# Kernel tuning notes

Hardware: AMD Instinct MI355X
Metric: run time of the kernel (lower is better)

## Reference

```python
import jax, jax.numpy as jnp
import numpy as np

N = 7          # N_AGENTS (hardcoded in source)
H = 4          # n_heads
TOP_K = 3
EPS = 1e-5
NEG = -1.0e9


def _gat(x, W, a_src, a_dst, edge_mask):
    # x: (B,N,F), W: (F,H*Hd), a_src/a_dst: (H,Hd), edge_mask: (N,N)
    B = x.shape[0]
    Hd = a_src.shape[1]
    h = (x @ W).reshape(B, N, H, Hd)
    s_src = jnp.einsum('bnhd,hd->bnh', h, a_src)
    s_dst = jnp.einsum('bnhd,hd->bnh', h, a_dst)
    e = s_src[:, :, None, :] + s_dst[:, None, :, :]          # (B,N,N,H)
    e = jnp.where(e > 0, e, 0.2 * e)                          # LeakyReLU(0.2)
    m = edge_mask[None, :, :, None]
    e = e * m + (1.0 - m) * NEG
    if TOP_K < N:
        # k-th largest along axis=2 (ascending sort -> index N-TOP_K)
        thr = jnp.sort(e, axis=2)[:, :, N - TOP_K:N - TOP_K + 1, :]
        sm = (e >= thr).astype(e.dtype)
        e = e * sm + (1.0 - sm) * NEG
    alpha = jax.nn.softmax(e, axis=2)
    alpha = jnp.nan_to_num(alpha)
    out = jnp.einsum('bijh,bjhd->bihd', alpha, h).reshape(B, N, H * Hd)
    return out, alpha.mean(-1)


def _ln(x, w, b):
    mu = x.mean(-1, keepdims=True)
    var = ((x - mu) ** 2).mean(-1, keepdims=True)
    return (x - mu) / jnp.sqrt(var + EPS) * w + b


def _forward(node_feats, context, base_preds, regime_feats, edge_logits,
             W1, a_src1, a_dst1, W2, a_src2, a_dst2,
             ln1_w, ln1_b, ln2_w, ln2_b, skip_w, skip_b,
             base_w1, base_b1, base_w2, base_b2,
             reg_w1, reg_b1, reg_w2, reg_b2,
             gate_w1, gate_b1, gate_w2, gate_b2,
             res_w1, res_b1, res_w2, res_b2):
    B = node_feats.shape[0]
    eye = jnp.eye(N, dtype=edge_logits.dtype)
    edge_mask = jax.nn.sigmoid(edge_logits) * (1.0 - eye) + eye

    skip = node_feats @ skip_w + skip_b
    h1, _ = _gat(node_feats, W1, a_src1, a_dst1, edge_mask)
    h = jax.nn.relu(_ln(h1 + skip, ln1_w, ln1_b))
    h2, attn = _gat(h, W2, a_src2, a_dst2, edge_mask)
    h = jax.nn.relu(_ln(h2 + h, ln2_w, ln2_b))

    combined = jnp.concatenate([h.reshape(B, -1), context], axis=-1)
    w_base = jax.nn.softmax(jax.nn.relu(combined @ base_w1 + base_b1) @ base_w2 + base_b2, axis=-1)
    w_regime = jax.nn.softmax(jax.nn.relu(combined @ reg_w1 + reg_b1) @ reg_w2 + reg_b2, axis=-1)
    gate = jax.nn.sigmoid(jnp.tanh(regime_feats @ gate_w1 + gate_b1) @ gate_w2 + gate_b2)  # (B,1)
    weights = (1.0 - gate) * w_base + gate * w_regime
    pred = (weights * base_preds).sum(-1)
    residual = (jnp.tanh(combined @ res_w1 + res_b1) @ res_w2 + res_b2)[:, 0] * 0.05
    pred = jnp.maximum(pred + residual, 0.05)
    return pred, weights, gate, edge_mask, attn


def setup_inputs() -> dict:
    key = jax.random.key(0)
    B, F, C, HID, NB = 16384, 256, 128, 256, 2
    Hd = HID // H
    G = N * HID + C
    ks = iter(jax.random.split(key, 40))
    nrm = lambda shp, s: jax.random.normal(next(ks), shp, jnp.float32) * s
    d = {
        'node_feats': nrm((B, N, F), 1.0),
        'context': nrm((B, C), 1.0),
        'base_preds': jax.random.uniform(next(ks), (B, NB), jnp.float32),
        'regime_feats': nrm((B, 3), 1.0),
        'edge_logits': nrm((N, N), 0.1),
        'W1': nrm((F, HID), (2.0 / (F + HID)) ** 0.5),
        'a_src1': nrm((H, Hd), 0.1), 'a_dst1': nrm((H, Hd), 0.1),
        'W2': nrm((HID, HID), (1.0 / HID) ** 0.5),
        'a_src2': nrm((H, Hd), 0.1), 'a_dst2': nrm((H, Hd), 0.1),
        'ln1_w': jnp.ones((HID,), jnp.float32), 'ln1_b': jnp.zeros((HID,), jnp.float32),
        'ln2_w': jnp.ones((HID,), jnp.float32), 'ln2_b': jnp.zeros((HID,), jnp.float32),
        'skip_w': nrm((F, HID), (1.0 / F) ** 0.5), 'skip_b': jnp.zeros((HID,), jnp.float32),
        'base_w1': nrm((G, 32), (1.0 / G) ** 0.5), 'base_b1': jnp.zeros((32,), jnp.float32),
        'base_w2': nrm((32, NB), 0.1), 'base_b2': jnp.zeros((NB,), jnp.float32),
        'reg_w1': nrm((G, 32), (1.0 / G) ** 0.5), 'reg_b1': jnp.zeros((32,), jnp.float32),
        'reg_w2': nrm((32, NB), 0.1), 'reg_b2': jnp.zeros((NB,), jnp.float32),
        'gate_w1': nrm((3, 8), 0.5), 'gate_b1': jnp.zeros((8,), jnp.float32),
        'gate_w2': nrm((8, 1), 0.3), 'gate_b2': jnp.zeros((1,), jnp.float32),
        'res_w1': nrm((G, 16), (1.0 / G) ** 0.5), 'res_b1': jnp.zeros((16,), jnp.float32),
        'res_w2': nrm((16, 1), 0.2), 'res_b2': jnp.zeros((1,), jnp.float32),
    }
    return d


def reference(node_feats, context, base_preds, regime_feats, edge_logits,
              W1, a_src1, a_dst1, W2, a_src2, a_dst2,
              ln1_w, ln1_b, ln2_w, ln2_b, skip_w, skip_b,
              base_w1, base_b1, base_w2, base_b2,
              reg_w1, reg_b1, reg_w2, reg_b2,
              gate_w1, gate_b1, gate_w2, gate_b2,
              res_w1, res_b1, res_w2, res_b2):
    return _forward(node_feats, context, base_preds, regime_feats, edge_logits,
                    W1, a_src1, a_dst1, W2, a_src2, a_dst2,
                    ln1_w, ln1_b, ln2_w, ln2_b, skip_w, skip_b,
                    base_w1, base_b1, base_w2, base_b2,
                    reg_w1, reg_b1, reg_w2, reg_b2,
                    gate_w1, gate_b1, gate_w2, gate_b2,
                    res_w1, res_b1, res_w2, res_b2)
```

## Files before the change

### kernel.cpp

```cpp
#include <hip/hip_runtime.h>
#include <hip/hip_bf16.h>

typedef unsigned short u16;
typedef __attribute__((ext_vector_type(8))) short bfrag8;
typedef __attribute__((ext_vector_type(8))) unsigned short u16x8;
typedef __attribute__((ext_vector_type(4))) unsigned short u16x4;
typedef __attribute__((ext_vector_type(4))) float f32x4;

__device__ __forceinline__ float bf2f(u16 u) {
    union { unsigned int i; float f; } v; v.i = ((unsigned int)u) << 16; return v.f;
}
__device__ __forceinline__ u16 f2bf(float f) {
    union { __hip_bfloat16 h; u16 u; } cv;
    cv.h = __float2bfloat16(f);
    return cv.u;
}
__device__ __forceinline__ float fast_tanh(float x) {
    float e = __expf(2.f * x);
    return (e - 1.f) / (e + 1.f);
}

#define TILE_M 128
#define TILE_N 128
#define TILE_K 32

#define GLOAD_LDS16(g, l) \
    __builtin_amdgcn_global_load_lds( \
        (const __attribute__((address_space(1))) void*)(g), \
        (__attribute__((address_space(3))) void*)(l), 16, 0, 0)

template<int HAS_BIAS, int C_MODE, int NGUARD>
__global__ __launch_bounds__(256)
void gemm_k(const u16* __restrict__ A, const u16* __restrict__ Bt,
            const float* __restrict__ bias, void* __restrict__ Cp,
            int M, int N, int K, int lda, int ldc, int nt, int kchunk)
{
    __shared__ u16 As[2][TILE_M][TILE_K];
    __shared__ u16 Bs[2][TILE_N][TILE_K];

    const int nwg = gridDim.x;
    const int q = nwg >> 3, r = nwg & 7;
    const int xcd = blockIdx.x & 7, pos = blockIdx.x >> 3;
    const int wg = (xcd < r ? xcd * (q + 1) : r * (q + 1) + (xcd - r) * q) + pos;
    const int m0 = (wg / nt) * TILE_M;
    const int n0 = (wg % nt) * TILE_N;

    const int kc   = blockIdx.y;
    const int kbeg = kc * kchunk;
    const int kend = (kbeg + kchunk < K) ? kbeg + kchunk : K;

    const int t    = threadIdx.x;
    const int lane = t & 63;
    const int w    = t >> 6;
    const int wm   = (w >> 1) * 64;
    const int wn   = (w & 1) * 64;
    const int lr   = lane & 15;
    const int kg   = (lane >> 4) * 8;

    const int lrow = lane >> 2;
    const int lcol = (lane & 3) * 8;
    const u16* gA0 = A  + (size_t)(m0 + 32 * w + lrow) * lda + lcol;
    const u16* gA1 = gA0 + (size_t)16 * lda;
    const u16* gB0 = Bt + (size_t)(n0 + 32 * w + lrow) * K + lcol;
    const u16* gB1 = gB0 + (size_t)16 * K;
    char* lA = (char*)&As[0][0][0] + w * 2048;
    char* lB = (char*)&Bs[0][0][0] + w * 2048;

    f32x4 acc[4][4];
#pragma unroll
    for (int i = 0; i < 4; ++i)
#pragma unroll
        for (int j = 0; j < 4; ++j) acc[i][j] = (f32x4){0.f, 0.f, 0.f, 0.f};

#define ISSUE(bufo, k0v) { \
        GLOAD_LDS16(gA0 + (k0v), lA + (bufo)); \
        GLOAD_LDS16(gA1 + (k0v), lA + 1024 + (bufo)); \
        GLOAD_LDS16(gB0 + (k0v), lB + (bufo)); \
        GLOAD_LDS16(gB1 + (k0v), lB + 1024 + (bufo)); \
    }

    ISSUE(0, kbeg)
    int buf = 0;
    for (int k0 = kbeg; k0 < kend; k0 += TILE_K) {
        const bool more = (k0 + TILE_K) < kend;
        if (more) {
            ISSUE((buf ^ 1) * 8192, k0 + TILE_K);
            asm volatile("s_waitcnt vmcnt(4)" ::: "memory");
        } else {
            asm volatile("s_waitcnt vmcnt(0)" ::: "memory");
        }
        __syncthreads();

        bfrag8 af[4], bfr[4];
#pragma unroll
        for (int mi = 0; mi < 4; ++mi) af[mi]  = *(const bfrag8*)&As[buf][wm + mi * 16 + lr][kg];
#pragma unroll
        for (int ni = 0; ni < 4; ++ni) bfr[ni] = *(const bfrag8*)&Bs[buf][wn + ni * 16 + lr][kg];
#pragma unroll
        for (int mi = 0; mi < 4; ++mi)
#pragma unroll
            for (int ni = 0; ni < 4; ++ni)
                acc[mi][ni] = __builtin_amdgcn_mfma_f32_16x16x32_bf16(af[mi], bfr[ni], acc[mi][ni], 0, 0, 0);

        __syncthreads();
        buf ^= 1;
    }
#undef ISSUE

    float* Cf = (float*)Cp + (size_t)kc * M * ldc;
#pragma unroll
    for (int mi = 0; mi < 4; ++mi) {
#pragma unroll
        for (int ni = 0; ni < 4; ++ni) {
            int col = n0 + wn + ni * 16 + lr;
            if (!NGUARD || col < N) {
                int row = m0 + wm + mi * 16 + (lane >> 4) * 4;
                float bv = 0.f;
                if (HAS_BIAS && kc == 0) bv = bias[col];
#pragma unroll
                for (int rr = 0; rr < 4; ++rr) {
                    float v = acc[mi][ni][rr] + bv;
                    if (C_MODE == 0) ((u16*)Cp)[(size_t)(row + rr) * ldc + col] = f2bf(v);
                    else             Cf[(size_t)(row + rr) * ldc + col] = v;
                }
            }
        }
    }
}

__global__ __launch_bounds__(256)
void precast_k(const float* __restrict__ in, u16* __restrict__ out, int n8)
{
    int i = blockIdx.x * 256 + threadIdx.x;
    if (i >= n8) return;
    const float4* p = (const float4*)(in + (size_t)i * 8);
    float4 a = p[0], b = p[1];
    u16x8 v;
    v[0] = f2bf(a.x); v[1] = f2bf(a.y); v[2] = f2bf(a.z); v[3] = f2bf(a.w);
    v[4] = f2bf(b.x); v[5] = f2bf(b.y); v[6] = f2bf(b.z); v[7] = f2bf(b.w);
    *(u16x8*)(out + (size_t)i * 8) = v;
}

__global__ __launch_bounds__(256)
void score_k(const u16* __restrict__ hs, int ld,
             const float* __restrict__ a_src, const float* __restrict__ a_dst,
             float* __restrict__ scores, int Mrows)
{
    const int wid  = blockIdx.x * 4 + (threadIdx.x >> 6);
    const int lane = threadIdx.x & 63;
    if (wid >= Mrows) return;
    const u16* hp = hs + (size_t)wid * ld + lane * 4;
    u16x4 xv = *(const u16x4*)hp;
    float s1 = 0.f, s2 = 0.f;
#pragma unroll
    for (int k = 0; k < 4; ++k) {
        float x = bf2f(xv[k]);
        s1 = fmaf(x, a_src[lane * 4 + k], s1);
        s2 = fmaf(x, a_dst[lane * 4 + k], s2);
    }
#pragma unroll
    for (int off = 1; off < 16; off <<= 1) {
        s1 += __shfl_xor(s1, off);
        s2 += __shfl_xor(s2, off);
    }
    if ((lane & 15) == 0) {
        scores[(size_t)wid * 8 + (lane >> 4)] = s1;
        scores[(size_t)wid * 8 + 4 + (lane >> 4)] = s2;
    }
}

template<int WRITE_ATTN>
__global__ __launch_bounds__(256)
void alpha_k(const float* __restrict__ scores, const float* __restrict__ em2,
             float* __restrict__ alpha, float* __restrict__ attn_out)
{
    const int t = blockIdx.x * 256 + threadIdx.x;
    const int b = t >> 2;
    const int h = t & 3;

    float ssrc[7], sdst[7];
#pragma unroll
    for (int n = 0; n < 7; ++n) {
        ssrc[n] = scores[(size_t)(b * 7 + n) * 8 + h];
        sdst[n] = scores[(size_t)(b * 7 + n) * 8 + 4 + h];
    }

    float al[49];
#pragma unroll
    for (int i = 0; i < 7; ++i) {
        float e[7];
#pragma unroll
        for (int j = 0; j < 7; ++j) {
            float v = ssrc[i] + sdst[j];
            v = fmaxf(v, 0.2f * v);
            e[j] = fmaf(v, em2[(i * 7 + j) * 2], em2[(i * 7 + j) * 2 + 1]);
        }
        float a1 = -3e38f, b1 = -3e38f, c1 = -3e38f;
#pragma unroll
        for (int j = 0; j < 7; ++j) {
            float v = e[j];
            float t2 = fminf(a1, v); a1 = fmaxf(a1, v);
            float t3 = fminf(b1, t2); b1 = fmaxf(b1, t2);
            c1 = fmaxf(c1, t3);
        }
        float psum = 0.f;
        float p[7];
#pragma unroll
        for (int j = 0; j < 7; ++j) {
            float qv = (e[j] >= c1) ? __expf(e[j] - a1) : 0.f;
            p[j] = qv; psum += qv;
        }
        float inv = 1.f / psum;
#pragma unroll
        for (int j = 0; j < 7; ++j) al[i * 7 + j] = p[j] * inv;
    }

    float* ap = alpha + (size_t)t * 49;
#pragma unroll
    for (int j = 0; j < 49; ++j) ap[j] = al[j];

    if (WRITE_ATTN) {
#pragma unroll
        for (int j = 0; j < 49; ++j) {
            float m = al[j];
            m += __shfl_xor(m, 1);
            m += __shfl_xor(m, 2);
            if (h == 0) attn_out[(size_t)b * 49 + j] = 0.25f * m;
        }
    }
}

__global__ __launch_bounds__(256)
void gat_apply_k(const u16* __restrict__ hh, int ld_hh,
                 const u16* __restrict__ resid, int ld_res, int res_off,
                 const float* __restrict__ alpha,
                 const float* __restrict__ ln_w, const float* __restrict__ ln_b,
                 u16* __restrict__ outp, int out_bs)
{
    const int t = threadIdx.x;
    const int b = blockIdx.x * 4 + (t >> 6);
    const int l = t & 63;
    const int c = l * 4;
    const int h = l >> 4;
    const size_t rowbase = (size_t)b * 7;

    float hv[7][4];
#pragma unroll
    for (int n = 0; n < 7; ++n) {
        u16x4 qv = *(const u16x4*)&hh[(rowbase + n) * ld_hh + c];
#pragma unroll
        for (int k = 0; k < 4; ++k) hv[n][k] = bf2f(qv[k]);
    }

    const float* ap = alpha + ((size_t)b * 4 + h) * 49;
    float4 lw = *(const float4*)&ln_w[c];
    float4 lb = *(const float4*)&ln_b[c];

#pragma unroll
    for (int i = 0; i < 7; ++i) {
        float a0 = ap[i * 7 + 0], a1 = ap[i * 7 + 1], a2 = ap[i * 7 + 2],
              a3 = ap[i * 7 + 3], a4 = ap[i * 7 + 4], a5 = ap[i * 7 + 5],
              a6 = ap[i * 7 + 6];
        u16x4 rr = *(const u16x4*)&resid[(rowbase + i) * ld_res + res_off + c];
        float x[4];
#pragma unroll
        for (int k = 0; k < 4; ++k) {
            float pv = a0 * hv[0][k];
            pv = fmaf(a1, hv[1][k], pv);
            pv = fmaf(a2, hv[2][k], pv);
            pv = fmaf(a3, hv[3][k], pv);
            pv = fmaf(a4, hv[4][k], pv);
            pv = fmaf(a5, hv[5][k], pv);
            pv = fmaf(a6, hv[6][k], pv);
            x[k] = pv + bf2f(rr[k]);
        }
        float s1 = (x[0] + x[1]) + (x[2] + x[3]);
        float s2 = fmaf(x[0], x[0], x[1] * x[1]) + fmaf(x[2], x[2], x[3] * x[3]);
#pragma unroll
        for (int off = 32; off > 0; off >>= 1) {
            s1 += __shfl_xor(s1, off);
            s2 += __shfl_xor(s2, off);
        }
        float mu  = s1 * (1.f / 256.f);
        float var = fmaxf(s2 * (1.f / 256.f) - mu * mu, 0.f);
        float inv = rsqrtf(var + 1e-5f);
        u16x4 o;
        o[0] = f2bf(fmaxf((x[0] - mu) * inv * lw.x + lb.x, 0.f));
        o[1] = f2bf(fmaxf((x[1] - mu) * inv * lw.y + lb.y, 0.f));
        o[2] = f2bf(fmaxf((x[2] - mu) * inv * lw.z + lb.z, 0.f));
        o[3] = f2bf(fmaxf((x[3] - mu) * inv * lw.w + lb.w, 0.f));
        *(u16x4*)&outp[(size_t)b * out_bs + i * 256 + c] = o;
    }
}

__global__ __launch_bounds__(256)
void prep_k(const float* __restrict__ W1, const float* __restrict__ skip_w, const float* __restrict__ W2,
            const float* __restrict__ base_w1, const float* __restrict__ reg_w1, const float* __restrict__ res_w1,
            const float* __restrict__ skip_b, const float* __restrict__ base_b1, const float* __restrict__ reg_b1,
            const float* __restrict__ res_b1, const float* __restrict__ edge_logits,
            u16* __restrict__ Wt1, u16* __restrict__ Wt2, u16* __restrict__ Wt3,
            float* __restrict__ bias1, float* __restrict__ bias3,
            float* __restrict__ em2, float* __restrict__ em_out)
{
    int idx = blockIdx.x * 256 + threadIdx.x;
    if (idx < 512 * 256) {
        int n = idx >> 8, k = idx & 255;
        float v = (n < 256) ? W1[k * 256 + n] : skip_w[k * 256 + (n - 256)];
        Wt1[n * 256 + k] = f2bf(v); return;
    }
    idx -= 512 * 256;
    if (idx < 256 * 256) {
        int n = idx >> 8, k = idx & 255;
        Wt2[n * 256 + k] = f2bf(W2[k * 256 + n]); return;
    }
    idx -= 256 * 256;
    if (idx < 128 * 1920) {
        int n = idx / 1920, k = idx % 1920;
        float v = (n < 32) ? base_w1[k * 32 + n]
                : (n < 64) ? reg_w1[k * 32 + (n - 32)]
                : (n < 80) ? res_w1[k * 16 + (n - 64)] : 0.f;
        Wt3[n * 1920 + k] = f2bf(v); return;
    }
    idx -= 128 * 1920;
    if (idx < 512) { bias1[idx] = (idx < 256) ? 0.f : skip_b[idx - 256]; return; }
    idx -= 512;
    if (idx < 80) {
        bias3[idx] = (idx < 32) ? base_b1[idx] : (idx < 64) ? reg_b1[idx - 32] : res_b1[idx - 64];
        return;
    }
    idx -= 80;
    if (idx < 49) {
        int i = idx / 7, j = idx % 7;
        float s = 1.f / (1.f + __expf(-edge_logits[idx]));
        float m = (i == j) ? 1.f : s;
        em2[idx * 2] = m;
        em2[idx * 2 + 1] = (1.f - m) * (-1e9f);
        em_out[idx] = m;
    }
}

__global__ __launch_bounds__(256)
void ctx_k(const float* __restrict__ ctx, u16* __restrict__ comb)
{
    int idx = blockIdx.x * 256 + threadIdx.x;
    int b = idx >> 7, cc = idx & 127;
    comb[(size_t)b * 1920 + 1792 + cc] = f2bf(ctx[idx]);
}

__global__ __launch_bounds__(64)
void head_finish(const float* __restrict__ ho,
                 const float* __restrict__ bp, const float* __restrict__ rf,
                 const float* __restrict__ bw2, const float* __restrict__ bb2,
                 const float* __restrict__ rw2, const float* __restrict__ rb2,
                 const float* __restrict__ gw1, const float* __restrict__ gb1,
                 const float* __restrict__ gw2, const float* __restrict__ gb2,
                 const float* __restrict__ resw2, const float* __restrict__ resb2,
                 float* __restrict__ out_pred, float* __restrict__ out_w, float* __restrict__ out_gate, int B)
{
    int b = blockIdx.x * 64 + threadIdx.x;
    if (b >= B) return;
    const size_t ss = (size_t)B * 80;
    const float* p = ho + (size_t)b * 80;

    float z0 = bb2[0], z1 = bb2[1];
#pragma unroll
    for (int j = 0; j < 32; j += 4) {
        float4 a0 = *(const float4*)(p + j);
        float4 a1 = *(const float4*)(p + ss + j);
        float4 a2 = *(const float4*)(p + 2 * ss + j);
        float4 a3 = *(const float4*)(p + 3 * ss + j);
        float v;
        v = fmaxf((a0.x + a1.x) + (a2.x + a3.x), 0.f); z0 = fmaf(v, bw2[2*j+0], z0); z1 = fmaf(v, bw2[2*j+1], z1);
        v = fmaxf((a0.y + a1.y) + (a2.y + a3.y), 0.f); z0 = fmaf(v, bw2[2*j+2], z0); z1 = fmaf(v, bw2[2*j+3], z1);
        v = fmaxf((a0.z + a1.z) + (a2.z + a3.z), 0.f); z0 = fmaf(v, bw2[2*j+4], z0); z1 = fmaf(v, bw2[2*j+5], z1);
        v = fmaxf((a0.w + a1.w) + (a2.w + a3.w), 0.f); z0 = fmaf(v, bw2[2*j+6], z0); z1 = fmaf(v, bw2[2*j+7], z1);
    }
    float mz = fmaxf(z0, z1); float e0 = __expf(z0 - mz), e1 = __expf(z1 - mz); float inv = 1.f / (e0 + e1);
    float wb0 = e0 * inv, wb1 = e1 * inv;

    z0 = rb2[0]; z1 = rb2[1];
#pragma unroll
    for (int j = 0; j < 32; j += 4) {
        float4 a0 = *(const float4*)(p + 32 + j);
        float4 a1 = *(const float4*)(p + ss + 32 + j);
        float4 a2 = *(const float4*)(p + 2 * ss + 32 + j);
        float4 a3 = *(const float4*)(p + 3 * ss + 32 + j);
        float v;
        v = fmaxf((a0.x + a1.x) + (a2.x + a3.x), 0.f); z0 = fmaf(v, rw2[2*j+0], z0); z1 = fmaf(v, rw2[2*j+1], z1);
        v = fmaxf((a0.y + a1.y) + (a2.y + a3.y), 0.f); z0 = fmaf(v, rw2[2*j+2], z0); z1 = fmaf(v, rw2[2*j+3], z1);
        v = fmaxf((a0.z + a1.z) + (a2.z + a3.z), 0.f); z0 = fmaf(v, rw2[2*j+4], z0); z1 = fmaf(v, rw2[2*j+5], z1);
        v = fmaxf((a0.w + a1.w) + (a2.w + a3.w), 0.f); z0 = fmaf(v, rw2[2*j+6], z0); z1 = fmaf(v, rw2[2*j+7], z1);
    }
    mz = fmaxf(z0, z1); e0 = __expf(z0 - mz); e1 = __expf(z1 - mz); inv = 1.f / (e0 + e1);
    float wr0 = e0 * inv, wr1 = e1 * inv;

    float r = resb2[0];
#pragma unroll
    for (int j = 0; j < 16; j += 4) {
        float4 a0 = *(const float4*)(p + 64 + j);
        float4 a1 = *(const float4*)(p + ss + 64 + j);
        float4 a2 = *(const float4*)(p + 2 * ss + 64 + j);
        float4 a3 = *(const float4*)(p + 3 * ss + 64 + j);
        r = fmaf(fast_tanh((a0.x + a1.x) + (a2.x + a3.x)), resw2[j + 0], r);
        r = fmaf(fast_tanh((a0.y + a1.y) + (a2.y + a3.y)), resw2[j + 1], r);
        r = fmaf(fast_tanh((a0.z + a1.z) + (a2.z + a3.z)), resw2[j + 2], r);
        r = fmaf(fast_tanh((a0.w + a1.w) + (a2.w + a3.w)), resw2[j + 3], r);
    }

    float g = gb2[0];
#pragma unroll
    for (int j = 0; j < 8; ++j) {
        float a = gb1[j];
#pragma unroll
        for (int i = 0; i < 3; ++i) a += rf[(size_t)b * 3 + i] * gw1[i * 8 + j];
        g += fast_tanh(a) * gw2[j];
    }
    float gg = 1.f / (1.f + __expf(-g));
    float w0 = (1.f - gg) * wb0 + gg * wr0;
    float w1 = (1.f - gg) * wb1 + gg * wr1;
    float pred = w0 * bp[(size_t)b * 2] + w1 * bp[(size_t)b * 2 + 1];
    pred = fmaxf(pred + r * 0.05f, 0.05f);
    out_pred[b] = pred;
    out_w[(size_t)b * 2] = w0; out_w[(size_t)b * 2 + 1] = w1;
    out_gate[b] = gg;
}

extern "C" void kernel_launch(void* const* d_in, const int* in_sizes, int n_in,
                              void* d_out, int out_size, void* d_ws, size_t ws_size,
                              hipStream_t stream)
{
    const int B = in_sizes[1] / 128;
    const int Mbig = B * 7;

    const float* node_feats   = (const float*)d_in[0];
    const float* context      = (const float*)d_in[1];
    const float* base_preds   = (const float*)d_in[2];
    const float* regime_feats = (const float*)d_in[3];
    const float* edge_logits  = (const float*)d_in[4];
    const float* W1      = (const float*)d_in[5];
    const float* a_src1  = (const float*)d_in[6];
    const float* a_dst1  = (const float*)d_in[7];
    const float* W2      = (const float*)d_in[8];
    const float* a_src2  = (const float*)d_in[9];
    const float* a_dst2  = (const float*)d_in[10];
    const float* ln1_w   = (const float*)d_in[11];
    const float* ln1_b   = (const float*)d_in[12];
    const float* ln2_w   = (const float*)d_in[13];
    const float* ln2_b   = (const float*)d_in[14];
    const float* skip_w  = (const float*)d_in[15];
    const float* skip_b  = (const float*)d_in[16];
    const float* base_w1 = (const float*)d_in[17];
    const float* base_b1 = (const float*)d_in[18];
    const float* base_w2 = (const float*)d_in[19];
    const float* base_b2 = (const float*)d_in[20];
    const float* reg_w1  = (const float*)d_in[21];
    const float* reg_b1  = (const float*)d_in[22];
    const float* reg_w2  = (const float*)d_in[23];
    const float* reg_b2  = (const float*)d_in[24];
    const float* gate_w1 = (const float*)d_in[25];
    const float* gate_b1 = (const float*)d_in[26];
    const float* gate_w2 = (const float*)d_in[27];
    const float* gate_b2 = (const float*)d_in[28];
    const float* res_w1  = (const float*)d_in[29];
    const float* res_b1  = (const float*)d_in[30];
    const float* res_w2  = (const float*)d_in[31];
    const float* res_b2  = (const float*)d_in[32];

    char* ws = (char*)d_ws;
    size_t off = 0;
    u16* hs1 = (u16*)(ws + off);
    u16* hh2 = (u16*)(ws + off);
    off += (size_t)Mbig * 512 * 2;
    u16* hbuf = (u16*)(ws + off);  off += (size_t)Mbig * 256 * 2;
    u16* comb = (u16*)(ws + off);  off += (size_t)B * 1920 * 2;
    u16* nf_bf = comb;
    float* headout = (float*)(ws + off); off += (size_t)4 * B * 80 * 4;
    u16* Wt1 = (u16*)(ws + off); off += 512 * 256 * 2;
    u16* Wt2 = (u16*)(ws + off); off += 256 * 256 * 2;
    u16* Wt3 = (u16*)(ws + off); off += (size_t)128 * 1920 * 2;
    float* bias1 = (float*)(ws + off); off += 512 * 4;
    float* bias3 = (float*)(ws + off); off += 128 * 4;
    float* em2   = (float*)(ws + off); off += 128 * 4;
    float* scoresb = (float*)(ws + off); off += (size_t)Mbig * 8 * 4;
    float* alphab  = (float*)(ws + off); off += (size_t)B * 4 * 49 * 4;

    float* out_pred = (float*)d_out;
    float* out_w    = out_pred + B;
    float* out_gate = out_pred + 3 * (size_t)B;
    float* out_em   = out_pred + 4 * (size_t)B;
    float* out_attn = out_pred + 4 * (size_t)B + 49;

    const int B4blocks = (B * 4) / 256;

    {
        int n8 = Mbig * 256 / 8;
        precast_k<<<dim3((n8 + 255) / 256), dim3(256), 0, stream>>>(node_feats, nf_bf, n8);
    }

    prep_k<<<dim3(1731), dim3(256), 0, stream>>>(W1, skip_w, W2, base_w1, reg_w1, res_w1,
        skip_b, base_b1, reg_b1, res_b1, edge_logits, Wt1, Wt2, Wt3, bias1, bias3, em2, out_em);

    gemm_k<1, 0, 0><<<dim3((Mbig / 128) * 4, 1), dim3(256), 0, stream>>>(
        nf_bf, Wt1, bias1, (void*)hs1, Mbig, 512, 256, 256, 512, 4, 256);

    score_k<<<dim3(Mbig / 4), dim3(256), 0, stream>>>(hs1, 512, a_src1, a_dst1, scoresb, Mbig);

    alpha_k<0><<<dim3(B4blocks), dim3(256), 0, stream>>>(scoresb, em2, alphab, (float*)nullptr);

    gat_apply_k<<<dim3(B / 4), dim3(256), 0, stream>>>(
        hs1, 512, hs1, 512, 256, alphab, ln1_w, ln1_b, hbuf, 1792);

    gemm_k<0, 0, 0><<<dim3((Mbig / 128) * 2, 1), dim3(256), 0, stream>>>(
        hbuf, Wt2, (const float*)nullptr, (void*)hh2, Mbig, 256, 256, 256, 256, 2, 256);

    score_k<<<dim3(Mbig / 4), dim3(256), 0, stream>>>(hh2, 256, a_src2, a_dst2, scoresb, Mbig);

    alpha_k<1><<<dim3(B4blocks), dim3(256), 0, stream>>>(scoresb, em2, alphab, out_attn);

    gat_apply_k<<<dim3(B / 4), dim3(256), 0, stream>>>(
        hh2, 256, hbuf, 256, 0, alphab, ln2_w, ln2_b, comb, 1920);

    ctx_k<<<dim3(B * 128 / 256), dim3(256), 0, stream>>>(context, comb);

    gemm_k<1, 1, 1><<<dim3(B / 128, 4), dim3(256), 0, stream>>>(
        comb, Wt3, bias3, (void*)headout, B, 80, 1920, 1920, 80, 1, 480);

    head_finish<<<dim3((B + 63) / 64), dim3(64), 0, stream>>>(
        headout, base_preds, regime_feats, base_w2, base_b2, reg_w2, reg_b2,
        gate_w1, gate_b1, gate_w2, gate_b2, res_w2, res_b2, out_pred, out_w, out_gate, B);
}
```

Before: 289.1 us.

## Single-buffer GEMM LDS, merge precast into prep, fuse context cast into GAT apply

Removes the double-buffered LDS prefetch from the GEMM, so each K-step now loads, waits on vmcnt(0), then computes. The input precast is merged into the prep kernel and the context bf16 cast into the second gat_apply, cutting two kernel launches. Halving LDS may allow more resident workgroups, but global load latency is no longer overlapped with MFMA work.

```diff
diff --git a/kernel.cpp b/kernel.cpp
--- a/kernel.cpp
+++ b/kernel.cpp
@@ -35,8 +35,8 @@
             const float* __restrict__ bias, void* __restrict__ Cp,
             int M, int N, int K, int lda, int ldc, int nt, int kchunk)
 {
-    __shared__ u16 As[2][TILE_M][TILE_K];
-    __shared__ u16 Bs[2][TILE_N][TILE_K];
+    __shared__ u16 As[TILE_M][TILE_K];
+    __shared__ u16 Bs[TILE_N][TILE_K];
 
     const int nwg = gridDim.x;
     const int q = nwg >> 3, r = nwg & 7;
@@ -63,8 +63,10 @@
     const u16* gA1 = gA0 + (size_t)16 * lda;
     const u16* gB0 = Bt + (size_t)(n0 + 32 * w + lrow) * K + lcol;
     const u16* gB1 = gB0 + (size_t)16 * K;
-    char* lA = (char*)&As[0][0][0] + w * 2048;
-    char* lB = (char*)&Bs[0][0][0] + w * 2048;
+    char* lA0 = (char*)&As[0][0] + w * 2048;
+    char* lA1 = lA0 + 1024;
+    char* lB0 = (char*)&Bs[0][0] + w * 2048;
+    char* lB1 = lB0 + 1024;
 
     f32x4 acc[4][4];
 #pragma unroll
@@ -72,30 +74,19 @@
 #pragma unroll
         for (int j = 0; j < 4; ++j) acc[i][j] = (f32x4){0.f, 0.f, 0.f, 0.f};
 
-#define ISSUE(bufo, k0v) { \
-        GLOAD_LDS16(gA0 + (k0v), lA + (bufo)); \
-        GLOAD_LDS16(gA1 + (k0v), lA + 1024 + (bufo)); \
-        GLOAD_LDS16(gB0 + (k0v), lB + (bufo)); \
-        GLOAD_LDS16(gB1 + (k0v), lB + 1024 + (bufo)); \
-    }
-
-    ISSUE(0, kbeg)
-    int buf = 0;
     for (int k0 = kbeg; k0 < kend; k0 += TILE_K) {
-        const bool more = (k0 + TILE_K) < kend;
-        if (more) {
-            ISSUE((buf ^ 1) * 8192, k0 + TILE_K);
-            asm volatile("s_waitcnt vmcnt(4)" ::: "memory");
-        } else {
-            asm volatile("s_waitcnt vmcnt(0)" ::: "memory");
-        }
+        GLOAD_LDS16(gA0 + k0, lA0);
+        GLOAD_LDS16(gA1 + k0, lA1);
+        GLOAD_LDS16(gB0 + k0, lB0);
+        GLOAD_LDS16(gB1 + k0, lB1);
+        asm volatile("s_waitcnt vmcnt(0)" ::: "memory");
         __syncthreads();
 
         bfrag8 af[4], bfr[4];
 #pragma unroll
-        for (int mi = 0; mi < 4; ++mi) af[mi]  = *(const bfrag8*)&As[buf][wm + mi * 16 + lr][kg];
-#pragma unroll
-        for (int ni = 0; ni < 4; ++ni) bfr[ni] = *(const bfrag8*)&Bs[buf][wn + ni * 16 + lr][kg];
+        for (int mi = 0; mi < 4; ++mi) af[mi]  = *(const bfrag8*)&As[wm + mi * 16 + lr][kg];
+#pragma unroll
+        for (int ni = 0; ni < 4; ++ni) bfr[ni] = *(const bfrag8*)&Bs[wn + ni * 16 + lr][kg];
 #pragma unroll
         for (int mi = 0; mi < 4; ++mi)
 #pragma unroll
@@ -103,9 +94,7 @@
                 acc[mi][ni] = __builtin_amdgcn_mfma_f32_16x16x32_bf16(af[mi], bfr[ni], acc[mi][ni], 0, 0, 0);
 
         __syncthreads();
-        buf ^= 1;
-    }
-#undef ISSUE
+    }
 
     float* Cf = (float*)Cp + (size_t)kc * M * ldc;
 #pragma unroll
@@ -129,19 +118,6 @@
 }
 
 __global__ __launch_bounds__(256)
-void precast_k(const float* __restrict__ in, u16* __restrict__ out, int n8)
-{
-    int i = blockIdx.x * 256 + threadIdx.x;
-    if (i >= n8) return;
-    const float4* p = (const float4*)(in + (size_t)i * 8);
-    float4 a = p[0], b = p[1];
-    u16x8 v;
-    v[0] = f2bf(a.x); v[1] = f2bf(a.y); v[2] = f2bf(a.z); v[3] = f2bf(a.w);
-    v[4] = f2bf(b.x); v[5] = f2bf(b.y); v[6] = f2bf(b.z); v[7] = f2bf(b.w);
-    *(u16x8*)(out + (size_t)i * 8) = v;
-}
-
-__global__ __launch_bounds__(256)
 void score_k(const u16* __restrict__ hs, int ld,
              const float* __restrict__ a_src, const float* __restrict__ a_dst,
              float* __restrict__ scores, int Mrows)
@@ -230,12 +206,14 @@
     }
 }
 
+template<int CTX>
 __global__ __launch_bounds__(256)
 void gat_apply_k(const u16* __restrict__ hh, int ld_hh,
                  const u16* __restrict__ resid, int ld_res, int res_off,
                  const float* __restrict__ alpha,
                  const float* __restrict__ ln_w, const float* __restrict__ ln_b,
-                 u16* __restrict__ outp, int out_bs)
+                 u16* __restrict__ outp, int out_bs,
+                 const float* __restrict__ ctx)
 {
     const int t = threadIdx.x;
     const int b = blockIdx.x * 4 + (t >> 6);
@@ -291,18 +269,37 @@
         o[3] = f2bf(fmaxf((x[3] - mu) * inv * lw.w + lb.w, 0.f));
         *(u16x4*)&outp[(size_t)b * out_bs + i * 256 + c] = o;
     }
+
+    if (CTX) {
+        float2 cv = *(const float2*)&ctx[(size_t)b * 128 + l * 2];
+        u16 c0 = f2bf(cv.x), c1 = f2bf(cv.y);
+        u16* cp = outp + (size_t)b * out_bs + 1792 + l * 2;
+        cp[0] = c0; cp[1] = c1;
+    }
 }
 
 __global__ __launch_bounds__(256)
-void prep_k(const float* __restrict__ W1, const float* __restrict__ skip_w, const float* __restrict__ W2,
-            const float* __restrict__ base_w1, const float* __restrict__ reg_w1, const float* __restrict__ res_w1,
-            const float* __restrict__ skip_b, const float* __restrict__ base_b1, const float* __restrict__ reg_b1,
-            const float* __restrict__ res_b1, const float* __restrict__ edge_logits,
-            u16* __restrict__ Wt1, u16* __restrict__ Wt2, u16* __restrict__ Wt3,
-            float* __restrict__ bias1, float* __restrict__ bias3,
-            float* __restrict__ em2, float* __restrict__ em_out)
-{
-    int idx = blockIdx.x * 256 + threadIdx.x;
+void prep_all_k(const float* __restrict__ nf, u16* __restrict__ nf_bf, int n8, int npre,
+                const float* __restrict__ W1, const float* __restrict__ skip_w, const float* __restrict__ W2,
+                const float* __restrict__ base_w1, const float* __restrict__ reg_w1, const float* __restrict__ res_w1,
+                const float* __restrict__ skip_b, const float* __restrict__ base_b1, const float* __restrict__ reg_b1,
+                const float* __restrict__ res_b1, const float* __restrict__ edge_logits,
+                u16* __restrict__ Wt1, u16* __restrict__ Wt2, u16* __restrict__ Wt3,
+                float* __restrict__ bias1, float* __restrict__ bias3,
+                float* __restrict__ em2, float* __restrict__ em_out)
+{
+    if ((int)blockIdx.x < npre) {
+        int i = blockIdx.x * 256 + threadIdx.x;
+        if (i >= n8) return;
+        const float4* p = (const float4*)(nf + (size_t)i * 8);
+        float4 a = p[0], b = p[1];
+        u16x8 v;
+        v[0] = f2bf(a.x); v[1] = f2bf(a.y); v[2] = f2bf(a.z); v[3] = f2bf(a.w);
+        v[4] = f2bf(b.x); v[5] = f2bf(b.y); v[6] = f2bf(b.z); v[7] = f2bf(b.w);
+        *(u16x8*)(nf_bf + (size_t)i * 8) = v;
+        return;
+    }
+    int idx = (blockIdx.x - npre) * 256 + threadIdx.x;
     if (idx < 512 * 256) {
         int n = idx >> 8, k = idx & 255;
         float v = (n < 256) ? W1[k * 256 + n] : skip_w[k * 256 + (n - 256)];
@@ -337,14 +334,6 @@
         em2[idx * 2 + 1] = (1.f - m) * (-1e9f);
         em_out[idx] = m;
     }
-}
-
-__global__ __launch_bounds__(256)
-void ctx_k(const float* __restrict__ ctx, u16* __restrict__ comb)
-{
-    int idx = blockIdx.x * 256 + threadIdx.x;
-    int b = idx >> 7, cc = idx & 127;
-    comb[(size_t)b * 1920 + 1792 + cc] = f2bf(ctx[idx]);
 }
 
 __global__ __launch_bounds__(64)
@@ -494,11 +483,13 @@
 
     {
         int n8 = Mbig * 256 / 8;
-        precast_k<<<dim3((n8 + 255) / 256), dim3(256), 0, stream>>>(node_feats, nf_bf, n8);
-    }
-
-    prep_k<<<dim3(1731), dim3(256), 0, stream>>>(W1, skip_w, W2, base_w1, reg_w1, res_w1,
-        skip_b, base_b1, reg_b1, res_b1, edge_logits, Wt1, Wt2, Wt3, bias1, bias3, em2, out_em);
+        int npre = (n8 + 255) / 256;
+        prep_all_k<<<dim3(npre + 1731), dim3(256), 0, stream>>>(
+            node_feats, nf_bf, n8, npre,
+            W1, skip_w, W2, base_w1, reg_w1, res_w1,
+            skip_b, base_b1, reg_b1, res_b1, edge_logits,
+            Wt1, Wt2, Wt3, bias1, bias3, em2, out_em);
+    }
 
     gemm_k<1, 0, 0><<<dim3((Mbig / 128) * 4, 1), dim3(256), 0, stream>>>(
         nf_bf, Wt1, bias1, (void*)hs1, Mbig, 512, 256, 256, 512, 4, 256);
@@ -507,8 +498,8 @@
 
     alpha_k<0><<<dim3(B4blocks), dim3(256), 0, stream>>>(scoresb, em2, alphab, (float*)nullptr);
 
-    gat_apply_k<<<dim3(B / 4), dim3(256), 0, stream>>>(
-        hs1, 512, hs1, 512, 256, alphab, ln1_w, ln1_b, hbuf, 1792);
+    gat_apply_k<0><<<dim3(B / 4), dim3(256), 0, stream>>>(
+        hs1, 512, hs1, 512, 256, alphab, ln1_w, ln1_b, hbuf, 1792, (const float*)nullptr);
 
     gemm_k<0, 0, 0><<<dim3((Mbig / 128) * 2, 1), dim3(256), 0, stream>>>(
         hbuf, Wt2, (const float*)nullptr, (void*)hh2, Mbig, 256, 256, 256, 256, 2, 256);
@@ -517,10 +508,8 @@
 
     alpha_k<1><<<dim3(B4blocks), dim3(256), 0, stream>>>(scoresb, em2, alphab, out_attn);
 
-    gat_apply_k<<<dim3(B / 4), dim3(256), 0, stream>>>(
-        hh2, 256, hbuf, 256, 0, alphab, ln2_w, ln2_b, comb, 1920);
-
-    ctx_k<<<dim3(B * 128 / 256), dim3(256), 0, stream>>>(context, comb);
+    gat_apply_k<1><<<dim3(B / 4), dim3(256), 0, stream>>>(
+        hh2, 256, hbuf, 256, 0, alphab, ln2_w, ln2_b, comb, 1920, context);
 
     gemm_k<1, 1, 1><<<dim3(B / 128, 4), dim3(256), 0, stream>>>(
         comb, Wt3, bias3, (void*)headout, B, 80, 1920, 1920, 80, 1, 480);
```

After: 287.7 us (median of 2 runs). About the same (-0.5%).
